# Optimization experiments

Hardware: AMD Instinct MI355X
Metric: run time of the kernel (lower is better)

The kernel has to match this reference:

```python
import jax, jax.numpy as jnp
import numpy as np

NUM_EXPERTS = 64
HIDDEN = 4096
TOP_K = 2
B, S = 4, 4096


def setup_inputs() -> dict:
    key = jax.random.key(0)
    k1, k2 = jax.random.split(key)
    hidden_states = jax.random.normal(k1, (B, S, HIDDEN), dtype=jnp.float32)
    W = jax.random.normal(k2, (NUM_EXPERTS, HIDDEN), dtype=jnp.float32) * 0.02
    return {"hidden_states": hidden_states, "W": W}


def reference(hidden_states, W):
    # router logits: [B, S, E]
    logits = jnp.einsum("bsh,eh->bse", hidden_states, W)
    flat = logits.reshape(-1, NUM_EXPERTS)  # [T, E]
    # top-k routing (z-loss / aux-loss do not change forward values; they only
    # inject gradients via the custom autograd function in the torch original)
    scores, top_indices = jax.lax.top_k(flat, TOP_K)  # [T, K] each
    return (scores.reshape(B, S, TOP_K), top_indices.reshape(B, S, TOP_K))
```

## Files before the change

### kernel.cpp

```cpp
#include <hip/hip_runtime.h>
#include <hip/hip_bf16.h>
#include <math.h>

#define NUM_EXPERTS 64
#define HIDDEN      4096
#define T_TOKENS    16384

using short8 = __attribute__((ext_vector_type(8))) short;
using f32x4  = __attribute__((ext_vector_type(4))) float;

__device__ __forceinline__ unsigned pack_pair(float f0, float f1, unsigned& lopk) {
    __hip_bfloat162 h2 = __float22bfloat162_rn(make_float2(f0, f1));
    unsigned hb; __builtin_memcpy(&hb, &h2, 4);
    float h0 = __builtin_bit_cast(float, hb << 16);
    float h1 = __builtin_bit_cast(float, hb & 0xffff0000u);
    __hip_bfloat162 l2 = __float22bfloat162_rn(make_float2(f0 - h0, f1 - h1));
    unsigned lb; __builtin_memcpy(&lb, &l2, 4);
    lopk = lb;
    return hb;
}
__device__ __forceinline__ void split8(const float4 a, const float4 b, uint4& hi, uint4& lo) {
    hi.x = pack_pair(a.x, a.y, lo.x);
    hi.y = pack_pair(a.z, a.w, lo.y);
    hi.z = pack_pair(b.x, b.y, lo.z);
    hi.w = pack_pair(b.z, b.w, lo.w);
}

#define MFMA(a, b, c) __builtin_amdgcn_mfma_f32_16x16x32_bf16((a), (b), (c), 0, 0, 0)

__global__ __launch_bounds__(256) void w_split_kernel(
    const float* __restrict__ W, unsigned char* __restrict__ ws)
{
    const int j  = blockIdx.x * 256 + threadIdx.x;
    const int l  = j & 63;
    const int nt = (j >> 6) & 3;
    const int t  = j >> 8;
    const int e  = nt * 16 + (l & 15);
    const int k0 = t * 32 + ((l >> 4) & 3) * 8;
    const float* p = W + (size_t)e * HIDDEN + k0;
    float4 w0 = *reinterpret_cast<const float4*>(p);
    float4 w1 = *reinterpret_cast<const float4*>(p + 4);
    uint4 hi, lo;
    split8(w0, w1, hi, lo);
    *reinterpret_cast<uint4*>(ws + (size_t)j * 16)            = hi;
    *reinterpret_cast<uint4*>(ws + 524288 + (size_t)j * 16)   = lo;
}


#define LOAD_A4(dst, t_) do {                                                  \
    const float* pA_ = aBase + (size_t)(t_) * 32;                              \
    _Pragma("unroll")                                                          \
    for (int mt_ = 0; mt_ < 4; ++mt_) {                                        \
        dst[mt_][0] = *reinterpret_cast<const float4*>(pA_ + (size_t)mt_ * 16 * HIDDEN);     \
        dst[mt_][1] = *reinterpret_cast<const float4*>(pA_ + (size_t)mt_ * 16 * HIDDEN + 4); \
    } } while (0)

#define LOAD_W(dst, t_) do {                                                   \
    const unsigned char* pW_ = wsHi + (size_t)(tBase + (t_)) * 4096 + laneOff; \
    _Pragma("unroll")                                                          \
    for (int nt_ = 0; nt_ < 4; ++nt_) {                                        \
        dst[nt_]     = *reinterpret_cast<const uint4*>(pW_ + nt_ * 1024);      \
        dst[nt_ + 4] = *reinterpret_cast<const uint4*>(pW_ + 524288 + nt_ * 1024); \
    } } while (0)

#define CHUNK4(ab_, wb_) do {                                                  \
    _Pragma("unroll")                                                          \
    for (int mt_ = 0; mt_ < 4; ++mt_) {                                        \
        uint4 hi_, lo_;                                                        \
        split8(ab_[mt_][0], ab_[mt_][1], hi_, lo_);                            \
        short8 ah_ = __builtin_bit_cast(short8, hi_);                          \
        short8 al_ = __builtin_bit_cast(short8, lo_);                          \
        _Pragma("unroll")                                                      \
        for (int nt_ = 0; nt_ < 4; ++nt_) {                                    \
            short8 wh_ = __builtin_bit_cast(short8, wb_[nt_]);                 \
            short8 wl_ = __builtin_bit_cast(short8, wb_[nt_ + 4]);             \
            acc[mt_][nt_] = MFMA(ah_, wh_, acc[mt_][nt_]);                     \
            acc[mt_][nt_] = MFMA(ah_, wl_, acc[mt_][nt_]);                     \
            acc[mt_][nt_] = MFMA(al_, wh_, acc[mt_][nt_]);                     \
        } } } while (0)

__global__ __launch_bounds__(512, 2) void router_mfma_topk(
    const float* __restrict__ A,
    const unsigned char* __restrict__ wsHi,
    float* __restrict__ out)
{
    __shared__ f32x4 part[4][4][4][64];

    const int tid  = threadIdx.x;
    const int lane = tid & 63;
    const int w    = tid >> 6;
    const int tok0 = blockIdx.x * 64;
    const int tBase = w * 16;

    const float* aBase = A + (size_t)(tok0 + (lane & 15)) * HIDDEN
                           + w * 512 + ((lane >> 4) & 3) * 8;
    const int laneOff = lane * 16;

    f32x4 acc[4][4];
#pragma unroll
    for (int mt = 0; mt < 4; ++mt)
#pragma unroll
        for (int nt = 0; nt < 4; ++nt) acc[mt][nt] = (f32x4){0.f, 0.f, 0.f, 0.f};

    float4 aC[4][2], aN[4][2];
    uint4  wX[8], wY[8];

    LOAD_W(wX, 0);
    LOAD_A4(aC, 0);

#pragma unroll
    for (int t = 0; t < 16; t += 2) {
        LOAD_W(wY, t + 1);
        LOAD_A4(aN, t + 1);
        CHUNK4(aC, wX);
        if (t + 2 < 16) { LOAD_W(wX, t + 2); LOAD_A4(aC, t + 2); }
        CHUNK4(aN, wY);
    }

    if (w < 4) {
#pragma unroll
        for (int mt = 0; mt < 4; ++mt)
#pragma unroll
            for (int nt = 0; nt < 4; ++nt) part[w][mt][nt][lane] = acc[mt][nt];
    }
    __syncthreads();
    if (w >= 4) {
#pragma unroll
        for (int mt = 0; mt < 4; ++mt)
#pragma unroll
            for (int nt = 0; nt < 4; ++nt)
                part[w - 4][mt][nt][lane] = part[w - 4][mt][nt][lane] + acc[mt][nt];
    }
    __syncthreads();

    if (w < 4) {
        f32x4 s[4];
#pragma unroll
        for (int nt = 0; nt < 4; ++nt) {
            s[nt] = part[0][w][nt][lane];
#pragma unroll
            for (int q = 1; q < 4; ++q) s[nt] = s[nt] + part[q][w][nt][lane];
        }

        const int eBase = lane & 15;
#pragma unroll
        for (int r = 0; r < 4; ++r) {
            float b1 = s[0][r]; int i1 = eBase;
            float b2 = -INFINITY; int i2 = 0;
#pragma unroll
            for (int nt = 1; nt < 4; ++nt) {
                float v = s[nt][r];
                int   e = nt * 16 + eBase;
                if (v > b1)      { b2 = b1; i2 = i1; b1 = v; i1 = e; }
                else if (v > b2) { b2 = v;  i2 = e; }
            }
#pragma unroll
            for (int m = 1; m <= 8; m <<= 1) {
                float o1 = __shfl_xor(b1, m); int oi1 = __shfl_xor(i1, m);
                float o2 = __shfl_xor(b2, m); int oi2 = __shfl_xor(i2, m);
                float n1, c, n2; int ni1, ci, ni2;
                if (o1 > b1 || (o1 == b1 && oi1 < i1)) { n1 = o1; ni1 = oi1; c = b1; ci = i1; }
                else                                   { n1 = b1; ni1 = i1;  c = o1; ci = oi1; }
                if (b2 > o2 || (b2 == o2 && i2 < oi2)) { n2 = b2; ni2 = i2; }
                else                                   { n2 = o2; ni2 = oi2; }
                if (c > n2 || (c == n2 && ci < ni2))   { n2 = c;  ni2 = ci; }
                b1 = n1; i1 = ni1; b2 = n2; i2 = ni2;
            }
            if ((lane & 15) == 0) {
                const int tok = tok0 + w * 16 + (lane >> 4) * 4 + r;
                out[(size_t)tok * 2 + 0] = b1;
                out[(size_t)tok * 2 + 1] = b2;
                out[(size_t)2 * T_TOKENS + (size_t)tok * 2 + 0] = (float)i1;
                out[(size_t)2 * T_TOKENS + (size_t)tok * 2 + 1] = (float)i2;
            }
        }
    }
}

extern "C" void kernel_launch(void* const* d_in, const int* in_sizes, int n_in,
                              void* d_out, int out_size, void* d_ws, size_t ws_size,
                              hipStream_t stream) {
    const float* A = (const float*)d_in[0];
    const float* W = (const float*)d_in[1];
    float* out = (float*)d_out;
    unsigned char* ws = (unsigned char*)d_ws;

    w_split_kernel<<<dim3(128), dim3(256), 0, stream>>>(W, ws);
    router_mfma_topk<<<dim3(T_TOKENS / 64), dim3(512), 0, stream>>>(A, ws, out);
}
```

Baseline: 69.14 us.

## Split K across blocks with W slice staged in LDS and separate top-k combine

The fused GEMM+top-k kernel becomes a split-K GEMM. Each block copies a 128KB hi/lo bf16 slice of W into LDS once and computes 512 tokens over one eighth of the hidden dimension. Partial logits go to a global workspace, and a new combine kernel sums the eight partials per token and does a serial top-2 scan. This removes repeated W reads from L2 and the in-block cross-wave reduction. The cost is 128KB of LDS per block, which limits occupancy, extra global write and read traffic for the partials, a third kernel launch, and poorly coalesced per-thread reads in the combine kernel.

```diff
diff --git a/kernel.cpp b/kernel.cpp
--- a/kernel.cpp
+++ b/kernel.cpp
@@ -5,6 +5,8 @@
 #define NUM_EXPERTS 64
 #define HIDDEN      4096
 #define T_TOKENS    16384
+#define KSPLIT      8
+#define TOKB        512
 
 using short8 = __attribute__((ext_vector_type(8))) short;
 using f32x4  = __attribute__((ext_vector_type(4))) float;
@@ -55,12 +57,12 @@
         dst[mt_][1] = *reinterpret_cast<const float4*>(pA_ + (size_t)mt_ * 16 * HIDDEN + 4); \
     } } while (0)
 
-#define LOAD_W(dst, t_) do {                                                   \
-    const unsigned char* pW_ = wsHi + (size_t)(tBase + (t_)) * 4096 + laneOff; \
+#define LDSW(dst, t_) do {                                                     \
+    const unsigned char* pW_ = wlds + (size_t)(t_) * 4096 + laneOff;           \
     _Pragma("unroll")                                                          \
     for (int nt_ = 0; nt_ < 4; ++nt_) {                                        \
         dst[nt_]     = *reinterpret_cast<const uint4*>(pW_ + nt_ * 1024);      \
-        dst[nt_ + 4] = *reinterpret_cast<const uint4*>(pW_ + 524288 + nt_ * 1024); \
+        dst[nt_ + 4] = *reinterpret_cast<const uint4*>(pW_ + 65536 + nt_ * 1024); \
     } } while (0)
 
 #define CHUNK4(ab_, wb_) do {                                                  \
@@ -79,21 +81,35 @@
             acc[mt_][nt_] = MFMA(al_, wh_, acc[mt_][nt_]);                     \
         } } } while (0)
 
-__global__ __launch_bounds__(512, 2) void router_mfma_topk(
+__global__ __launch_bounds__(512, 2) void gemm_partial(
     const float* __restrict__ A,
     const unsigned char* __restrict__ wsHi,
-    float* __restrict__ out)
+    float* __restrict__ part)
 {
-    __shared__ f32x4 part[4][4][4][64];
+    __shared__ unsigned char wlds[131072];
 
     const int tid  = threadIdx.x;
     const int lane = tid & 63;
     const int w    = tid >> 6;
-    const int tok0 = blockIdx.x * 64;
-    const int tBase = w * 16;
+    const int ky   = blockIdx.y;
+    const int tok0 = blockIdx.x * TOKB + w * 64;
+
+    {
+        const unsigned char* srcH = wsHi + (size_t)ky * 65536;
+        const unsigned char* srcL = wsHi + 524288 + (size_t)ky * 65536;
+#pragma unroll
+        for (int i = 0; i < 8; ++i) {
+            const int off = (i * 512 + tid) * 16;
+            *reinterpret_cast<uint4*>(&wlds[off]) =
+                *reinterpret_cast<const uint4*>(&srcH[off]);
+            *reinterpret_cast<uint4*>(&wlds[65536 + off]) =
+                *reinterpret_cast<const uint4*>(&srcL[off]);
+        }
+    }
+    __syncthreads();
 
     const float* aBase = A + (size_t)(tok0 + (lane & 15)) * HIDDEN
-                           + w * 512 + ((lane >> 4) & 3) * 8;
+                           + ky * 512 + ((lane >> 4) & 3) * 8;
     const int laneOff = lane * 16;
 
     f32x4 acc[4][4];
@@ -102,79 +118,77 @@
 #pragma unroll
         for (int nt = 0; nt < 4; ++nt) acc[mt][nt] = (f32x4){0.f, 0.f, 0.f, 0.f};
 
-    float4 aC[4][2], aN[4][2];
-    uint4  wX[8], wY[8];
-
-    LOAD_W(wX, 0);
-    LOAD_A4(aC, 0);
-
-#pragma unroll
-    for (int t = 0; t < 16; t += 2) {
-        LOAD_W(wY, t + 1);
-        LOAD_A4(aN, t + 1);
-        CHUNK4(aC, wX);
-        if (t + 2 < 16) { LOAD_W(wX, t + 2); LOAD_A4(aC, t + 2); }
-        CHUNK4(aN, wY);
-    }
-
-    if (w < 4) {
-#pragma unroll
-        for (int mt = 0; mt < 4; ++mt)
-#pragma unroll
-            for (int nt = 0; nt < 4; ++nt) part[w][mt][nt][lane] = acc[mt][nt];
-    }
-    __syncthreads();
-    if (w >= 4) {
-#pragma unroll
-        for (int mt = 0; mt < 4; ++mt)
-#pragma unroll
-            for (int nt = 0; nt < 4; ++nt)
-                part[w - 4][mt][nt][lane] = part[w - 4][mt][nt][lane] + acc[mt][nt];
-    }
-    __syncthreads();
-
-    if (w < 4) {
-        f32x4 s[4];
+    float4 aX[4][2], aY[4][2];
+    uint4  wP[8], wQ[8];
+
+    LOAD_A4(aX, 0);
+    LDSW(wP, 0);
+
+    LOAD_A4(aY, 1);   LDSW(wQ, 1);   CHUNK4(aX, wP);
+    LOAD_A4(aX, 2);   LDSW(wP, 2);   CHUNK4(aY, wQ);
+    LOAD_A4(aY, 3);   LDSW(wQ, 3);   CHUNK4(aX, wP);
+    LOAD_A4(aX, 4);   LDSW(wP, 4);   CHUNK4(aY, wQ);
+    LOAD_A4(aY, 5);   LDSW(wQ, 5);   CHUNK4(aX, wP);
+    LOAD_A4(aX, 6);   LDSW(wP, 6);   CHUNK4(aY, wQ);
+    LOAD_A4(aY, 7);   LDSW(wQ, 7);   CHUNK4(aX, wP);
+    LOAD_A4(aX, 8);   LDSW(wP, 8);   CHUNK4(aY, wQ);
+    LOAD_A4(aY, 9);   LDSW(wQ, 9);   CHUNK4(aX, wP);
+    LOAD_A4(aX, 10);  LDSW(wP, 10);  CHUNK4(aY, wQ);
+    LOAD_A4(aY, 11);  LDSW(wQ, 11);  CHUNK4(aX, wP);
+    LOAD_A4(aX, 12);  LDSW(wP, 12);  CHUNK4(aY, wQ);
+    LOAD_A4(aY, 13);  LDSW(wQ, 13);  CHUNK4(aX, wP);
+    LOAD_A4(aX, 14);  LDSW(wP, 14);  CHUNK4(aY, wQ);
+    LOAD_A4(aY, 15);  LDSW(wQ, 15);  CHUNK4(aX, wP);
+                                     CHUNK4(aY, wQ);
+
+#pragma unroll
+    for (int mt = 0; mt < 4; ++mt) {
 #pragma unroll
         for (int nt = 0; nt < 4; ++nt) {
-            s[nt] = part[0][w][nt][lane];
-#pragma unroll
-            for (int q = 1; q < 4; ++q) s[nt] = s[nt] + part[q][w][nt][lane];
-        }
-
-        const int eBase = lane & 15;
-#pragma unroll
-        for (int r = 0; r < 4; ++r) {
-            float b1 = s[0][r]; int i1 = eBase;
-            float b2 = -INFINITY; int i2 = 0;
-#pragma unroll
-            for (int nt = 1; nt < 4; ++nt) {
-                float v = s[nt][r];
-                int   e = nt * 16 + eBase;
-                if (v > b1)      { b2 = b1; i2 = i1; b1 = v; i1 = e; }
-                else if (v > b2) { b2 = v;  i2 = e; }
-            }
-#pragma unroll
-            for (int m = 1; m <= 8; m <<= 1) {
-                float o1 = __shfl_xor(b1, m); int oi1 = __shfl_xor(i1, m);
-                float o2 = __shfl_xor(b2, m); int oi2 = __shfl_xor(i2, m);
-                float n1, c, n2; int ni1, ci, ni2;
-                if (o1 > b1 || (o1 == b1 && oi1 < i1)) { n1 = o1; ni1 = oi1; c = b1; ci = i1; }
-                else                                   { n1 = b1; ni1 = i1;  c = o1; ci = oi1; }
-                if (b2 > o2 || (b2 == o2 && i2 < oi2)) { n2 = b2; ni2 = i2; }
-                else                                   { n2 = o2; ni2 = oi2; }
-                if (c > n2 || (c == n2 && ci < ni2))   { n2 = c;  ni2 = ci; }
-                b1 = n1; i1 = ni1; b2 = n2; i2 = ni2;
-            }
-            if ((lane & 15) == 0) {
-                const int tok = tok0 + w * 16 + (lane >> 4) * 4 + r;
-                out[(size_t)tok * 2 + 0] = b1;
-                out[(size_t)tok * 2 + 1] = b2;
-                out[(size_t)2 * T_TOKENS + (size_t)tok * 2 + 0] = (float)i1;
-                out[(size_t)2 * T_TOKENS + (size_t)tok * 2 + 1] = (float)i2;
+            const int e = nt * 16 + (lane & 15);
+#pragma unroll
+            for (int r = 0; r < 4; ++r) {
+                const int tok = tok0 + mt * 16 + (lane >> 4) * 4 + r;
+                part[((size_t)tok * KSPLIT + ky) * 64 + e] = acc[mt][nt][r];
             }
         }
     }
+}
+
+__global__ __launch_bounds__(64) void combine_topk(
+    const float* __restrict__ part,
+    float* __restrict__ out)
+{
+    const int tok = blockIdx.x * 64 + threadIdx.x;
+    const float4* p = reinterpret_cast<const float4*>(part + (size_t)tok * KSPLIT * 64);
+
+    float s[64];
+#pragma unroll
+    for (int i = 0; i < 16; ++i) {
+        float4 v = p[i];
+        s[4*i+0] = v.x; s[4*i+1] = v.y; s[4*i+2] = v.z; s[4*i+3] = v.w;
+    }
+#pragma unroll
+    for (int sl = 1; sl < KSPLIT; ++sl) {
+#pragma unroll
+        for (int i = 0; i < 16; ++i) {
+            float4 v = p[sl * 16 + i];
+            s[4*i+0] += v.x; s[4*i+1] += v.y; s[4*i+2] += v.z; s[4*i+3] += v.w;
+        }
+    }
+
+    float b1 = -INFINITY, b2 = -INFINITY;
+    int i1 = 0, i2 = 0;
+#pragma unroll
+    for (int e = 0; e < NUM_EXPERTS; ++e) {
+        float v = s[e];
+        if (v > b1)      { b2 = b1; i2 = i1; b1 = v; i1 = e; }
+        else if (v > b2) { b2 = v;  i2 = e; }
+    }
+    out[(size_t)tok * 2 + 0] = b1;
+    out[(size_t)tok * 2 + 1] = b2;
+    out[(size_t)2 * T_TOKENS + (size_t)tok * 2 + 0] = (float)i1;
+    out[(size_t)2 * T_TOKENS + (size_t)tok * 2 + 1] = (float)i2;
 }
 
 extern "C" void kernel_launch(void* const* d_in, const int* in_sizes, int n_in,
@@ -184,7 +198,9 @@
     const float* W = (const float*)d_in[1];
     float* out = (float*)d_out;
     unsigned char* ws = (unsigned char*)d_ws;
+    float* part = reinterpret_cast<float*>(ws + (1 << 20));
 
     w_split_kernel<<<dim3(128), dim3(256), 0, stream>>>(W, ws);
-    router_mfma_topk<<<dim3(T_TOKENS / 64), dim3(512), 0, stream>>>(A, ws, out);
-}
+    gemm_partial<<<dim3(T_TOKENS / TOKB, KSPLIT), dim3(512), 0, stream>>>(A, ws, part);
+    combine_topk<<<dim3(T_TOKENS / 64), dim3(64), 0, stream>>>(part, out);
+}
```

After: 78.81 us. +14.0%, slower.

## Stage activation tiles through LDS via direct global-to-LDS loads

Applied to the files above, without the earlier changes.

Replaces the per-thread register double-buffering of activation loads with global_load_lds async copies into a double-buffered shared-memory region, read back before the bf16 split and MFMA. The aim is to free VGPRs and let global loads for the next chunk overlap compute without holding data in registers. It adds block-wide __syncthreads per half-step, requests 128 KB of static LDS (with launch_bounds(512,2) this would cap occupancy, possibly to one block per CU), and drops the unroll pragma on the main loop. Correctness relies on the global-to-LDS write layout matching the lane offset used in the LDS reads.

```diff
diff --git a/kernel.cpp b/kernel.cpp
--- a/kernel.cpp
+++ b/kernel.cpp
@@ -27,6 +27,11 @@
 }
 
 #define MFMA(a, b, c) __builtin_amdgcn_mfma_f32_16x16x32_bf16((a), (b), (c), 0, 0, 0)
+
+#define GLOAD16(g_, l_)                                                        \
+    __builtin_amdgcn_global_load_lds(                                          \
+        (__attribute__((address_space(1))) unsigned*)(void*)(g_),              \
+        (__attribute__((address_space(3))) unsigned*)(void*)(l_), 16, 0, 0)
 
 __global__ __launch_bounds__(256) void w_split_kernel(
     const float* __restrict__ W, unsigned char* __restrict__ ws)
@@ -47,14 +52,6 @@
 }
 
 
-#define LOAD_A4(dst, t_) do {                                                  \
-    const float* pA_ = aBase + (size_t)(t_) * 32;                              \
-    _Pragma("unroll")                                                          \
-    for (int mt_ = 0; mt_ < 4; ++mt_) {                                        \
-        dst[mt_][0] = *reinterpret_cast<const float4*>(pA_ + (size_t)mt_ * 16 * HIDDEN);     \
-        dst[mt_][1] = *reinterpret_cast<const float4*>(pA_ + (size_t)mt_ * 16 * HIDDEN + 4); \
-    } } while (0)
-
 #define LOAD_W(dst, t_) do {                                                   \
     const unsigned char* pW_ = wsHi + (size_t)(tBase + (t_)) * 4096 + laneOff; \
     _Pragma("unroll")                                                          \
@@ -63,11 +60,24 @@
         dst[nt_ + 4] = *reinterpret_cast<const uint4*>(pW_ + 524288 + nt_ * 1024); \
     } } while (0)
 
-#define CHUNK4(ab_, wb_) do {                                                  \
+#define STAGE_A(b_, t_) do {                                                   \
+    unsigned char* ld_ = smem + (size_t)w * 16384 + (b_) * 8192;               \
+    const float* g0_ = aBase + (size_t)(t_) * 32;                              \
     _Pragma("unroll")                                                          \
     for (int mt_ = 0; mt_ < 4; ++mt_) {                                        \
+        const float* g_ = g0_ + (size_t)mt_ * 16 * HIDDEN;                     \
+        GLOAD16(g_,     ld_ + mt_ * 2048);                                     \
+        GLOAD16(g_ + 4, ld_ + mt_ * 2048 + 1024);                              \
+    } } while (0)
+
+#define CHUNK_LDS(b_, wb_) do {                                                \
+    const unsigned char* ls_ = smem + (size_t)w * 16384 + (b_) * 8192 + laneOff; \
+    _Pragma("unroll")                                                          \
+    for (int mt_ = 0; mt_ < 4; ++mt_) {                                        \
+        float4 q0_ = *reinterpret_cast<const float4*>(ls_ + mt_ * 2048);       \
+        float4 q1_ = *reinterpret_cast<const float4*>(ls_ + mt_ * 2048 + 1024);\
         uint4 hi_, lo_;                                                        \
-        split8(ab_[mt_][0], ab_[mt_][1], hi_, lo_);                            \
+        split8(q0_, q1_, hi_, lo_);                                            \
         short8 ah_ = __builtin_bit_cast(short8, hi_);                          \
         short8 al_ = __builtin_bit_cast(short8, lo_);                          \
         _Pragma("unroll")                                                      \
@@ -84,7 +94,7 @@
     const unsigned char* __restrict__ wsHi,
     float* __restrict__ out)
 {
-    __shared__ f32x4 part[4][4][4][64];
+    __shared__ unsigned char smem[131072];
 
     const int tid  = threadIdx.x;
     const int lane = tid & 63;
@@ -102,20 +112,24 @@
 #pragma unroll
         for (int nt = 0; nt < 4; ++nt) acc[mt][nt] = (f32x4){0.f, 0.f, 0.f, 0.f};
 
-    float4 aC[4][2], aN[4][2];
-    uint4  wX[8], wY[8];
+    uint4 wX[8], wY[8];
 
     LOAD_W(wX, 0);
-    LOAD_A4(aC, 0);
-
-#pragma unroll
-    for (int t = 0; t < 16; t += 2) {
+    STAGE_A(0, 0);
+    __syncthreads();
+
+    for (int tt = 0; tt < 8; ++tt) {
+        const int t = tt * 2;
         LOAD_W(wY, t + 1);
-        LOAD_A4(aN, t + 1);
-        CHUNK4(aC, wX);
-        if (t + 2 < 16) { LOAD_W(wX, t + 2); LOAD_A4(aC, t + 2); }
-        CHUNK4(aN, wY);
-    }
+        STAGE_A(1, t + 1);
+        CHUNK_LDS(0, wX);
+        __syncthreads();
+        if (tt < 7) { LOAD_W(wX, t + 2); STAGE_A(0, t + 2); }
+        CHUNK_LDS(1, wY);
+        __syncthreads();
+    }
+
+    f32x4 (*part)[4][4][64] = reinterpret_cast<f32x4 (*)[4][4][64]>(smem);
 
     if (w < 4) {
 #pragma unroll
```

New measurement: 75.30 us. 8.9% more time.
